# Performance work log

Hardware: AMD Instinct MI355X
Metric: run time of the kernel (lower is better)

## Reference

```python
import jax, jax.numpy as jnp
import numpy as np

B, H, S, D = 2, 16, 2048, 64
DROPOUT_RATE = 0.1
NEG = -1000000000.0


def setup_inputs() -> dict:
    k = jax.random.key(0)
    kq, kk, kv, km = jax.random.split(k, 4)
    return {
        "query": jax.random.normal(kq, (B, H, S, D), dtype=jnp.float32),
        "key": jax.random.normal(kk, (B, H, S, D), dtype=jnp.float32),
        "value": jax.random.normal(kv, (B, H, S, D), dtype=jnp.float32),
        "mask": jax.random.randint(km, (B, 1, 1, S), 0, 2, dtype=jnp.int32),
    }


def reference(query, key, value, mask):
    d_k = query.shape[-1]
    # scores: [B,H,S,S]
    scores = jnp.einsum("bhqd,bhkd->bhqk", query, key) / jnp.sqrt(
        jnp.asarray(d_k, query.dtype))
    scores = jnp.where(mask == 0, jnp.asarray(NEG, scores.dtype), scores)
    p_attn = jax.nn.softmax(scores, axis=-1)
    # dropout (train mode, inverted scaling) with a fixed key for determinism
    keep = jax.random.bernoulli(jax.random.key(42), 1.0 - DROPOUT_RATE,
                                p_attn.shape)
    p_attn = jnp.where(keep, p_attn / (1.0 - DROPOUT_RATE), 0.0).astype(
        p_attn.dtype)
    out = jnp.einsum("bhqk,bhkd->bhqd", p_attn, value)
    return (out, p_attn)
```

## Files before the change

kernel.cpp:

```cpp
#include <hip/hip_runtime.h>
#include <stdint.h>

#define H_N 16
#define S_N 2048
#define D_N 64
#define QB  64
#define KT  64

typedef __attribute__((ext_vector_type(8))) __bf16 bf16x8;
typedef __attribute__((ext_vector_type(4))) float f32x4;

__device__ __forceinline__ unsigned short f2bf(float f) {
  uint32_t u = __float_as_uint(f);
  u += 0x7FFFu + ((u >> 16) & 1u);
  return (unsigned short)(u >> 16);
}

__device__ __forceinline__ uint2 tf2x32(uint32_t c0, uint32_t c1) {
  const uint32_t K0 = 0u, K1 = 42u, K2 = 0x1BD11BDAu ^ 42u;
  uint32_t x0 = c0 + K0, x1 = c1 + K1;
#define TFR(r) x0 += x1; x1 = __builtin_rotateleft32(x1, r); x1 ^= x0;
  TFR(13) TFR(15) TFR(26) TFR(6)
  x0 += K1; x1 += K2 + 1u;
  TFR(17) TFR(29) TFR(16) TFR(24)
  x0 += K2; x1 += K0 + 2u;
  TFR(13) TFR(15) TFR(26) TFR(6)
  x0 += K0; x1 += K1 + 3u;
  TFR(17) TFR(29) TFR(16) TFR(24)
  x0 += K1; x1 += K2 + 4u;
  TFR(13) TFR(15) TFR(26) TFR(6)
  x0 += K2; x1 += K0 + 5u;
#undef TFR
  return make_uint2(x0, x1);
}

__device__ __forceinline__ bool keep_bit(uint32_t j) {
  uint2 o = tf2x32(0u, j);
  return (((o.x ^ o.y) >> 9) < 0x733333u);
}

__device__ __forceinline__ void stageTile(const float* __restrict__ g,
                                          unsigned short* __restrict__ lds, int tid) {
  const int row = tid >> 2;
  const int c4  = tid & 3;
  const float4* s = (const float4*)(g + (tid << 4));
  float4 a = s[0], b = s[1], c = s[2], d = s[3];
  uint4 q0, q1;
  q0.x = (uint32_t)f2bf(a.x) | ((uint32_t)f2bf(a.y) << 16);
  q0.y = (uint32_t)f2bf(a.z) | ((uint32_t)f2bf(a.w) << 16);
  q0.z = (uint32_t)f2bf(b.x) | ((uint32_t)f2bf(b.y) << 16);
  q0.w = (uint32_t)f2bf(b.z) | ((uint32_t)f2bf(b.w) << 16);
  q1.x = (uint32_t)f2bf(c.x) | ((uint32_t)f2bf(c.y) << 16);
  q1.y = (uint32_t)f2bf(c.z) | ((uint32_t)f2bf(c.w) << 16);
  q1.z = (uint32_t)f2bf(d.x) | ((uint32_t)f2bf(d.y) << 16);
  q1.w = (uint32_t)f2bf(d.z) | ((uint32_t)f2bf(d.w) << 16);
  const int rs = row & 7;
  *(uint4*)&lds[row * 64 + (((c4 * 2)     ^ rs) << 3)] = q0;
  *(uint4*)&lds[row * 64 + (((c4 * 2 + 1) ^ rs) << 3)] = q1;
}

__device__ __forceinline__ void stageTileT(const float* __restrict__ g,
                                           unsigned short* __restrict__ lds, int tid) {
  const int key = tid >> 2;
  const int c4  = tid & 3;
  const float4* s = (const float4*)(g + (tid << 4));
  float4 v0 = s[0], v1 = s[1], v2 = s[2], v3 = s[3];
  const int kc = key >> 3, ke = key & 7;
#define WRT(e, val) { const int dd = c4 * 16 + (e); \
    lds[dd * 64 + (((kc ^ (dd & 7)) << 3) | ke)] = f2bf(val); }
  WRT(0,  v0.x) WRT(1,  v0.y) WRT(2,  v0.z) WRT(3,  v0.w)
  WRT(4,  v1.x) WRT(5,  v1.y) WRT(6,  v1.z) WRT(7,  v1.w)
  WRT(8,  v2.x) WRT(9,  v2.y) WRT(10, v2.z) WRT(11, v2.w)
  WRT(12, v3.x) WRT(13, v3.y) WRT(14, v3.z) WRT(15, v3.w)
#undef WRT
}

__global__ __launch_bounds__(256, 4)
void attn_fused(const float* __restrict__ Q, const float* __restrict__ K,
                const float* __restrict__ V, const int* __restrict__ mask,
                float* __restrict__ outO, float* __restrict__ outP) {
  __shared__ uint4 smemRaw[2048];
  unsigned short* const sbase = (unsigned short*)smemRaw;
  unsigned short* const sQ = sbase;
  unsigned short* const sK = sbase + 4096;
  unsigned short* const sV = sbase + 8192;
  unsigned short* const sP = sbase + 12288;

  const int tid = threadIdx.x;
  const int l   = tid & 63;
  const int w   = tid >> 6;
  const int bid = blockIdx.x;
  const int b   = bid & 1;
  const int h   = (bid >> 1) & (H_N - 1);
  const int qt  = bid >> 5;
  const int qBase = qt * QB;

  const int lrow = l & 15;
  const int lq4  = l >> 4;

  const size_t base = ((size_t)b * H_N + h) * (size_t)(S_N * D_N);
  const int* const maskRow = mask + b * S_N;

  stageTile(Q + base + (size_t)qBase * D_N, sQ, tid);
  __syncthreads();

  bf16x8 qf[2];
  {
    const int qrow = w * 16 + lrow;
#pragma unroll
    for (int ks = 0; ks < 2; ++ks) {
      const int cc = ks * 4 + lq4;
      qf[ks] = *(const bf16x8*)&sQ[qrow * 64 + ((cc ^ (qrow & 7)) << 3)];
    }
  }

  float minv[4];
  {
    float lsum[4] = {0.f, 0.f, 0.f, 0.f};
    for (int kt = 0; kt < S_N / KT; ++kt) {
      __syncthreads();
      stageTile(K + base + (size_t)(kt * KT) * D_N, sK, tid);
      __syncthreads();
#pragma unroll
      for (int n = 0; n < 4; ++n) {
        const int krow = n * 16 + lrow;
        f32x4 acc = {0.f, 0.f, 0.f, 0.f};
#pragma unroll
        for (int ks = 0; ks < 2; ++ks) {
          const int cc = ks * 4 + lq4;
          bf16x8 kf = *(const bf16x8*)&sK[krow * 64 + ((cc ^ (krow & 7)) << 3)];
          acc = __builtin_amdgcn_mfma_f32_16x16x32_bf16(qf[ks], kf, acc, 0, 0, 0);
        }
        const float mf = (float)maskRow[kt * KT + krow];
#pragma unroll
        for (int r = 0; r < 4; ++r)
          lsum[r] += mf * __expf(acc[r] * 0.125f - 20.0f);
      }
    }
#pragma unroll
    for (int r = 0; r < 4; ++r) {
      float v = lsum[r];
      v += __shfl_xor(v, 1);
      v += __shfl_xor(v, 2);
      v += __shfl_xor(v, 4);
      v += __shfl_xor(v, 8);
      minv[r] = (v > 0.f) ? ((1.0f / 0.9f) / v) : 0.f;
    }
  }

  f32x4 oacc[4];
#pragma unroll
  for (int n = 0; n < 4; ++n)
    oacc[n] = (f32x4){0.f, 0.f, 0.f, 0.f};

  const uint32_t qg = (uint32_t)(qBase + w * 16 + lq4 * 4);
  const size_t pBase = ((size_t)b * H_N + h) * (size_t)(S_N * S_N);
  const uint32_t jBase = (uint32_t)(b * H_N + h) * 4194304u + qg * 2048u;

  for (int kt = 0; kt < S_N / KT; ++kt) {
    __syncthreads();
    stageTile (K + base + (size_t)(kt * KT) * D_N, sK, tid);
    stageTileT(V + base + (size_t)(kt * KT) * D_N, sV, tid);
    __syncthreads();

#pragma unroll
    for (int n = 0; n < 4; ++n) {
      const int krow = n * 16 + lrow;
      f32x4 acc = {0.f, 0.f, 0.f, 0.f};
#pragma unroll
      for (int ks = 0; ks < 2; ++ks) {
        const int cc = ks * 4 + lq4;
        bf16x8 kf = *(const bf16x8*)&sK[krow * 64 + ((cc ^ (krow & 7)) << 3)];
        acc = __builtin_amdgcn_mfma_f32_16x16x32_bf16(qf[ks], kf, acc, 0, 0, 0);
      }
      const int kg = kt * KT + krow;
      const float mf = (float)maskRow[kg];
      const uint32_t j0 = jBase + (uint32_t)kg;
#pragma unroll
      for (int r = 0; r < 4; ++r) {
        const float pe = mf * __expf(acc[r] * 0.125f - 20.0f) * minv[r];
        const bool keep = keep_bit(j0 + (uint32_t)r * 2048u);
        const float pd = keep ? pe : 0.0f;
        __builtin_nontemporal_store(pd, &outP[pBase + (size_t)(qg + r) * S_N + (size_t)kg]);
        const int prow = w * 16 + lq4 * 4 + r;
        sP[prow * 64 + ((((krow >> 3) ^ (prow & 7)) << 3) | (krow & 7))] = f2bf(pd);
      }
    }
#pragma unroll
    for (int ks = 0; ks < 2; ++ks) {
      const int cc = ks * 4 + lq4;
      const int prow = w * 16 + lrow;
      bf16x8 af = *(const bf16x8*)&sP[prow * 64 + ((cc ^ (prow & 7)) << 3)];
#pragma unroll
      for (int n = 0; n < 4; ++n) {
        const int vrow = n * 16 + lrow;
        bf16x8 vf = *(const bf16x8*)&sV[vrow * 64 + ((cc ^ (vrow & 7)) << 3)];
        oacc[n] = __builtin_amdgcn_mfma_f32_16x16x32_bf16(af, vf, oacc[n], 0, 0, 0);
      }
    }
  }

#pragma unroll
  for (int n = 0; n < 4; ++n)
#pragma unroll
    for (int r = 0; r < 4; ++r) {
      const size_t off = (((size_t)b * H_N + h) * S_N + (size_t)(qg + r)) * D_N + n * 16 + lrow;
      __builtin_nontemporal_store(oacc[n][r], &outO[off]);
    }
}

extern "C" void kernel_launch(void* const* d_in, const int* in_sizes, int n_in,
                              void* d_out, int out_size, void* d_ws, size_t ws_size,
                              hipStream_t stream) {
  const float* Q   = (const float*)d_in[0];
  const float* K   = (const float*)d_in[1];
  const float* V   = (const float*)d_in[2];
  const int* mask  = (const int*)d_in[3];
  float* outO = (float*)d_out;
  float* outP = outO + (size_t)2 * H_N * S_N * D_N;
  hipLaunchKernelGGL(attn_fused, dim3(1024), dim3(256), 0, stream,
                     Q, K, V, mask, outO, outP);
}
```

Before: 369.0 us.

## Prefetch next K/V tiles into registers while computing current tile

Splits tile staging into a global-load step and an LDS-write step. The load for tile kt+1 is issued right after the barrier, so it is in flight while tile kt is computed, in both the normalisation pass and the main pass. This hides global-memory latency behind the MFMA and exp/RNG work. The cost is 16 to 32 extra VGPRs per thread, which may cut occupancy under launch_bounds(256,4) or cause spills.

```diff
diff --git a/kernel.cpp b/kernel.cpp
--- a/kernel.cpp
+++ b/kernel.cpp
@@ -39,39 +39,43 @@
   return (((o.x ^ o.y) >> 9) < 0x733333u);
 }
 
-__device__ __forceinline__ void stageTile(const float* __restrict__ g,
-                                          unsigned short* __restrict__ lds, int tid) {
+struct StageReg { float4 a, b, c, d; };
+
+__device__ __forceinline__ void stageLoad(const float* __restrict__ g, int tid,
+                                          StageReg& r) {
+  const float4* s = (const float4*)(g + (tid << 4));
+  r.a = s[0]; r.b = s[1]; r.c = s[2]; r.d = s[3];
+}
+
+__device__ __forceinline__ void stageWrite(const StageReg& r,
+                                           unsigned short* __restrict__ lds, int tid) {
   const int row = tid >> 2;
   const int c4  = tid & 3;
-  const float4* s = (const float4*)(g + (tid << 4));
-  float4 a = s[0], b = s[1], c = s[2], d = s[3];
   uint4 q0, q1;
-  q0.x = (uint32_t)f2bf(a.x) | ((uint32_t)f2bf(a.y) << 16);
-  q0.y = (uint32_t)f2bf(a.z) | ((uint32_t)f2bf(a.w) << 16);
-  q0.z = (uint32_t)f2bf(b.x) | ((uint32_t)f2bf(b.y) << 16);
-  q0.w = (uint32_t)f2bf(b.z) | ((uint32_t)f2bf(b.w) << 16);
-  q1.x = (uint32_t)f2bf(c.x) | ((uint32_t)f2bf(c.y) << 16);
-  q1.y = (uint32_t)f2bf(c.z) | ((uint32_t)f2bf(c.w) << 16);
-  q1.z = (uint32_t)f2bf(d.x) | ((uint32_t)f2bf(d.y) << 16);
-  q1.w = (uint32_t)f2bf(d.z) | ((uint32_t)f2bf(d.w) << 16);
+  q0.x = (uint32_t)f2bf(r.a.x) | ((uint32_t)f2bf(r.a.y) << 16);
+  q0.y = (uint32_t)f2bf(r.a.z) | ((uint32_t)f2bf(r.a.w) << 16);
+  q0.z = (uint32_t)f2bf(r.b.x) | ((uint32_t)f2bf(r.b.y) << 16);
+  q0.w = (uint32_t)f2bf(r.b.z) | ((uint32_t)f2bf(r.b.w) << 16);
+  q1.x = (uint32_t)f2bf(r.c.x) | ((uint32_t)f2bf(r.c.y) << 16);
+  q1.y = (uint32_t)f2bf(r.c.z) | ((uint32_t)f2bf(r.c.w) << 16);
+  q1.z = (uint32_t)f2bf(r.d.x) | ((uint32_t)f2bf(r.d.y) << 16);
+  q1.w = (uint32_t)f2bf(r.d.z) | ((uint32_t)f2bf(r.d.w) << 16);
   const int rs = row & 7;
   *(uint4*)&lds[row * 64 + (((c4 * 2)     ^ rs) << 3)] = q0;
   *(uint4*)&lds[row * 64 + (((c4 * 2 + 1) ^ rs) << 3)] = q1;
 }
 
-__device__ __forceinline__ void stageTileT(const float* __restrict__ g,
-                                           unsigned short* __restrict__ lds, int tid) {
+__device__ __forceinline__ void stageWriteT(const StageReg& r,
+                                            unsigned short* __restrict__ lds, int tid) {
   const int key = tid >> 2;
   const int c4  = tid & 3;
-  const float4* s = (const float4*)(g + (tid << 4));
-  float4 v0 = s[0], v1 = s[1], v2 = s[2], v3 = s[3];
   const int kc = key >> 3, ke = key & 7;
 #define WRT(e, val) { const int dd = c4 * 16 + (e); \
     lds[dd * 64 + (((kc ^ (dd & 7)) << 3) | ke)] = f2bf(val); }
-  WRT(0,  v0.x) WRT(1,  v0.y) WRT(2,  v0.z) WRT(3,  v0.w)
-  WRT(4,  v1.x) WRT(5,  v1.y) WRT(6,  v1.z) WRT(7,  v1.w)
-  WRT(8,  v2.x) WRT(9,  v2.y) WRT(10, v2.z) WRT(11, v2.w)
-  WRT(12, v3.x) WRT(13, v3.y) WRT(14, v3.z) WRT(15, v3.w)
+  WRT(0,  r.a.x) WRT(1,  r.a.y) WRT(2,  r.a.z) WRT(3,  r.a.w)
+  WRT(4,  r.b.x) WRT(5,  r.b.y) WRT(6,  r.b.z) WRT(7,  r.b.w)
+  WRT(8,  r.c.x) WRT(9,  r.c.y) WRT(10, r.c.z) WRT(11, r.c.w)
+  WRT(12, r.d.x) WRT(13, r.d.y) WRT(14, r.d.z) WRT(15, r.d.w)
 #undef WRT
 }
 
@@ -101,7 +105,11 @@
   const size_t base = ((size_t)b * H_N + h) * (size_t)(S_N * D_N);
   const int* const maskRow = mask + b * S_N;
 
-  stageTile(Q + base + (size_t)qBase * D_N, sQ, tid);
+  {
+    StageReg qreg;
+    stageLoad(Q + base + (size_t)qBase * D_N, tid, qreg);
+    stageWrite(qreg, sQ, tid);
+  }
   __syncthreads();
 
   bf16x8 qf[2];
@@ -117,10 +125,14 @@
   float minv[4];
   {
     float lsum[4] = {0.f, 0.f, 0.f, 0.f};
+    StageReg kreg;
+    stageLoad(K + base, tid, kreg);
     for (int kt = 0; kt < S_N / KT; ++kt) {
       __syncthreads();
-      stageTile(K + base + (size_t)(kt * KT) * D_N, sK, tid);
-      __syncthreads();
+      stageWrite(kreg, sK, tid);
+      __syncthreads();
+      if (kt + 1 < S_N / KT)
+        stageLoad(K + base + (size_t)((kt + 1) * KT) * D_N, tid, kreg);
 #pragma unroll
       for (int n = 0; n < 4; ++n) {
         const int krow = n * 16 + lrow;
@@ -157,45 +169,54 @@
   const size_t pBase = ((size_t)b * H_N + h) * (size_t)(S_N * S_N);
   const uint32_t jBase = (uint32_t)(b * H_N + h) * 4194304u + qg * 2048u;
 
-  for (int kt = 0; kt < S_N / KT; ++kt) {
-    __syncthreads();
-    stageTile (K + base + (size_t)(kt * KT) * D_N, sK, tid);
-    stageTileT(V + base + (size_t)(kt * KT) * D_N, sV, tid);
-    __syncthreads();
-
-#pragma unroll
-    for (int n = 0; n < 4; ++n) {
-      const int krow = n * 16 + lrow;
-      f32x4 acc = {0.f, 0.f, 0.f, 0.f};
+  {
+    StageReg kreg, vreg;
+    stageLoad(K + base, tid, kreg);
+    stageLoad(V + base, tid, vreg);
+    for (int kt = 0; kt < S_N / KT; ++kt) {
+      __syncthreads();
+      stageWrite (kreg, sK, tid);
+      stageWriteT(vreg, sV, tid);
+      __syncthreads();
+      if (kt + 1 < S_N / KT) {
+        stageLoad(K + base + (size_t)((kt + 1) * KT) * D_N, tid, kreg);
+        stageLoad(V + base + (size_t)((kt + 1) * KT) * D_N, tid, vreg);
+      }
+
+#pragma unroll
+      for (int n = 0; n < 4; ++n) {
+        const int krow = n * 16 + lrow;
+        f32x4 acc = {0.f, 0.f, 0.f, 0.f};
+#pragma unroll
+        for (int ks = 0; ks < 2; ++ks) {
+          const int cc = ks * 4 + lq4;
+          bf16x8 kf = *(const bf16x8*)&sK[krow * 64 + ((cc ^ (krow & 7)) << 3)];
+          acc = __builtin_amdgcn_mfma_f32_16x16x32_bf16(qf[ks], kf, acc, 0, 0, 0);
+        }
+        const int kg = kt * KT + krow;
+        const float mf = (float)maskRow[kg];
+        const uint32_t j0 = jBase + (uint32_t)kg;
+#pragma unroll
+        for (int r = 0; r < 4; ++r) {
+          const float pe = mf * __expf(acc[r] * 0.125f - 20.0f) * minv[r];
+          const bool keep = keep_bit(j0 + (uint32_t)r * 2048u);
+          const float pd = keep ? pe : 0.0f;
+          __builtin_nontemporal_store(pd, &outP[pBase + (size_t)(qg + r) * S_N + (size_t)kg]);
+          const int prow = w * 16 + lq4 * 4 + r;
+          sP[prow * 64 + ((((krow >> 3) ^ (prow & 7)) << 3) | (krow & 7))] = f2bf(pd);
+        }
+      }
 #pragma unroll
       for (int ks = 0; ks < 2; ++ks) {
         const int cc = ks * 4 + lq4;
-        bf16x8 kf = *(const bf16x8*)&sK[krow * 64 + ((cc ^ (krow & 7)) << 3)];
-        acc = __builtin_amdgcn_mfma_f32_16x16x32_bf16(qf[ks], kf, acc, 0, 0, 0);
-      }
-      const int kg = kt * KT + krow;
-      const float mf = (float)maskRow[kg];
-      const uint32_t j0 = jBase + (uint32_t)kg;
-#pragma unroll
-      for (int r = 0; r < 4; ++r) {
-        const float pe = mf * __expf(acc[r] * 0.125f - 20.0f) * minv[r];
-        const bool keep = keep_bit(j0 + (uint32_t)r * 2048u);
-        const float pd = keep ? pe : 0.0f;
-        __builtin_nontemporal_store(pd, &outP[pBase + (size_t)(qg + r) * S_N + (size_t)kg]);
-        const int prow = w * 16 + lq4 * 4 + r;
-        sP[prow * 64 + ((((krow >> 3) ^ (prow & 7)) << 3) | (krow & 7))] = f2bf(pd);
-      }
-    }
-#pragma unroll
-    for (int ks = 0; ks < 2; ++ks) {
-      const int cc = ks * 4 + lq4;
-      const int prow = w * 16 + lrow;
-      bf16x8 af = *(const bf16x8*)&sP[prow * 64 + ((cc ^ (prow & 7)) << 3)];
-#pragma unroll
-      for (int n = 0; n < 4; ++n) {
-        const int vrow = n * 16 + lrow;
-        bf16x8 vf = *(const bf16x8*)&sV[vrow * 64 + ((cc ^ (vrow & 7)) << 3)];
-        oacc[n] = __builtin_amdgcn_mfma_f32_16x16x32_bf16(af, vf, oacc[n], 0, 0, 0);
+        const int prow = w * 16 + lrow;
+        bf16x8 af = *(const bf16x8*)&sP[prow * 64 + ((cc ^ (prow & 7)) << 3)];
+#pragma unroll
+        for (int n = 0; n < 4; ++n) {
+          const int vrow = n * 16 + lrow;
+          bf16x8 vf = *(const bf16x8*)&sV[vrow * 64 + ((cc ^ (vrow & 7)) << 3)];
+          oacc[n] = __builtin_amdgcn_mfma_f32_16x16x32_bf16(af, vf, oacc[n], 0, 0, 0);
+        }
       }
     }
   }
```

Result: slower. 383.4 us (+3.9%).
